# Kernel tuning notes

Measured on AMD Instinct MI355X. Metric: run time of the kernel, lower is better.

The kernel has to match this reference:

```python
import jax, jax.numpy as jnp
import numpy as np

B = 128      # graphs
N = 32       # atoms per graph (fixed)
NODES = B * N
E = B * N * N  # fully-connected edges incl. self-loops
H = 256      # hidden_dim
TD = 128     # time_dim
TYPE = 100   # type_dim
NF = 10      # frac_emb_freq
EDGE_DIM = NF * 2 * 3 + 6  # 66
L = 4        # num_layers
EPS = 1e-5


def _edges():
    idx = jnp.arange(NODES).reshape(B, N)
    ei = jnp.broadcast_to(idx[:, :, None], (B, N, N)).reshape(-1)  # row (target)
    ej = jnp.broadcast_to(idx[:, None, :], (B, N, N)).reshape(-1)  # col (source)
    return ei, ej


def _layernorm(x, g, b):
    mu = jnp.mean(x, axis=-1, keepdims=True)
    var = jnp.mean((x - mu) ** 2, axis=-1, keepdims=True)
    return (x - mu) * jax.lax.rsqrt(var + EPS) * g + b


def setup_inputs() -> dict:
    key = jax.random.key(0)
    ks = jax.random.split(key, 32)
    p = lambda k, shp: (jax.random.normal(k, shp, dtype=jnp.float32) * 0.02)
    inp = {
        "t": jax.random.uniform(ks[0], (B,), dtype=jnp.float32),
        "atom_types": jax.random.normal(ks[1], (NODES, TYPE), dtype=jnp.float32),
        "frac_coords": jax.random.uniform(ks[2], (NODES, 3), dtype=jnp.float32),
        "l_polar": jax.random.normal(ks[3], (B, 6), dtype=jnp.float32),
        "node2graph": jnp.repeat(jnp.arange(B, dtype=jnp.int32), N),
        # type_smooth
        "Ws": p(ks[4], (TYPE, H)), "bs": jnp.zeros((H,), jnp.float32),
        # node_embedding
        "Wn": p(ks[5], (H + TD, H)), "bn": jnp.zeros((H,), jnp.float32),
        # per-layer params, stacked over L
        "ln_g": jnp.ones((L, H), jnp.float32), "ln_b": jnp.zeros((L, H), jnp.float32),
        "m1_W": p(ks[6], (L, 2 * H + EDGE_DIM, H)), "m1_b": jnp.zeros((L, H), jnp.float32),
        "m2_W": p(ks[7], (L, H, H)), "m2_b": jnp.zeros((L, H), jnp.float32),
        "a1_W": p(ks[8], (L, 2 * H, H)), "a1_b": jnp.zeros((L, H), jnp.float32),
        "a2_W": p(ks[9], (L, H, H)), "a2_b": jnp.zeros((L, H), jnp.float32),
        # final layer norm + readouts
        "fln_g": jnp.ones((H,), jnp.float32), "fln_b": jnp.zeros((H,), jnp.float32),
        "type_W": p(ks[10], (H, TYPE)), "type_b": jnp.zeros((TYPE,), jnp.float32),
        "polar_W": p(ks[11], (H, 6)),
        "frac_W": p(ks[12], (H, 3)),
    }
    return inp


def reference(t, atom_types, frac_coords, l_polar, node2graph,
              Ws, bs, Wn, bn, ln_g, ln_b, m1_W, m1_b, m2_W, m2_b,
              a1_W, a1_b, a2_W, a2_b, fln_g, fln_b, type_W, type_b,
              polar_W, frac_W):
    ei, ej = _edges()
    edge2graph = node2graph[ei]

    # ---- node features: type_smooth + sinusoidal time embedding ----
    half = TD // 2
    tfreq = jnp.exp(jnp.arange(half, dtype=jnp.float32) * (-np.log(10000.0) / (half - 1)))
    targ = t[:, None] * tfreq[None, :]                       # [B, half]
    time_emb = jnp.concatenate([jnp.sin(targ), jnp.cos(targ)], axis=-1)  # [B, TD]
    time_emb = jnp.repeat(time_emb, N, axis=0)               # [NODES, TD]
    type_emb = atom_types @ Ws + bs                           # [NODES, H]
    nf = jnp.concatenate([type_emb, time_emb], axis=-1) @ Wn + bn  # [NODES, H]

    # ---- edge features: sinusoidal frac-diff embedding + l_polar ----
    d = jnp.mod(frac_coords[ej] - frac_coords[ei], 1.0)       # [E, 3]
    ffreq = 2.0 * np.pi * jnp.arange(NF, dtype=jnp.float32)
    femb = (d[:, :, None] * ffreq[None, None, :]).reshape(E, NF * 3)
    femb = jnp.concatenate([jnp.sin(femb), jnp.cos(femb)], axis=-1)  # [E, 60]
    ef = jnp.concatenate([femb, l_polar[edge2graph]], axis=-1)       # [E, 66]

    # ---- GNN layers ----
    ones = jnp.ones((E,), jnp.float32)
    cnt = jax.ops.segment_sum(ones, ei, num_segments=NODES)          # [NODES]
    cnt = jnp.maximum(cnt, 1.0)[:, None]
    for i in range(L):
        h = _layernorm(nf, ln_g[i], ln_b[i])
        mij = jnp.concatenate([h[ei], h[ej], ef], axis=-1)           # [E, 2H+66]
        mij = jax.nn.silu(mij @ m1_W[i] + m1_b[i])
        mij = jax.nn.silu(mij @ m2_W[i] + m2_b[i])                   # [E, H]
        msg = jax.ops.segment_sum(mij, ei, num_segments=NODES) / cnt  # scatter-mean
        a = jnp.concatenate([nf, msg], axis=-1)
        a = jax.nn.silu(a @ a1_W[i] + a1_b[i])
        a = jax.nn.silu(a @ a2_W[i] + a2_b[i])
        nf = nf + a

    nf = _layernorm(nf, fln_g, fln_b)
    gsum = jax.ops.segment_sum(nf, node2graph, num_segments=B)
    gcnt = jnp.maximum(jax.ops.segment_sum(jnp.ones((NODES,), jnp.float32), node2graph, num_segments=B), 1.0)
    graph_features = gsum / gcnt[:, None]

    type_pred = nf @ type_W + type_b
    l_polar_pred = graph_features @ polar_W
    frac_coords_pred = nf @ frac_W
    return type_pred, l_polar_pred, frac_coords_pred
```

## Files before the change

### kernel.cpp

```cpp
#include <hip/hip_runtime.h>
#include <hip/hip_bf16.h>

typedef __attribute__((ext_vector_type(8))) short short8;
typedef __attribute__((ext_vector_type(4))) short short4v;
typedef __attribute__((ext_vector_type(4))) float float4v;
typedef __bf16 bf16x8 __attribute__((ext_vector_type(8)));

#define MFMA16(A,B,C) __builtin_amdgcn_mfma_f32_16x16x32_bf16( \
    __builtin_bit_cast(bf16x8,(A)), __builtin_bit_cast(bf16x8,(B)), (C), 0, 0, 0)

static __device__ __forceinline__ float bf2f(unsigned short b){
  unsigned u = ((unsigned)b) << 16; float f; __builtin_memcpy(&f,&u,sizeof(f)); return f;
}
static __device__ __forceinline__ unsigned short f2bf(float f){
  __bf16 h = (__bf16)f;
  return __builtin_bit_cast(unsigned short, h);
}
static __device__ __forceinline__ float siluf(float x){
  return x * __builtin_amdgcn_rcpf(1.0f + __expf(-x));
}
static __device__ __forceinline__ float ldf(const float* p, size_t i){ return p[i]; }
static __device__ __forceinline__ float ldf(const unsigned short* p, size_t i){ return bf2f(p[i]); }

__global__ __launch_bounds__(256) void k_gemm(
    const unsigned short* __restrict__ A, int lda,
    const unsigned short* __restrict__ Bp, int KT, int NT,
    const float* __restrict__ bias,
    float* __restrict__ outF, int ldoF,
    unsigned short* __restrict__ outH, int ldoH,
    const float* __restrict__ res,
    int Nc, int flags)
{
  const int w = threadIdx.x >> 6, lane = threadIdx.x & 63;
  const int l15 = lane & 15, q = lane >> 4;
  const int rowL = blockIdx.x * 64 + w * 16;
  const int colB = blockIdx.y * 64;
  const short8* pa = (const short8*)(A + (size_t)(rowL + l15) * lda);
  const short8* pb = (const short8*)Bp;
  float4v acc[4] = {};
  int ntc[4];
  #pragma unroll
  for (int i = 0; i < 4; ++i){ int t = (colB >> 4) + i; ntc[i] = t < NT ? t : NT - 1; }
  for (int kt = 0; kt < KT; ++kt){
    short8 a = pa[kt * 4 + q];
    #pragma unroll
    for (int i = 0; i < 4; ++i){
      short8 b = pb[(size_t)(kt * NT + ntc[i]) * 64 + lane];
      acc[i] = MFMA16(a, b, acc[i]);
    }
  }
  const bool doB = flags & 2, doS = flags & 1, doR = flags & 4;
  #pragma unroll
  for (int i = 0; i < 4; ++i){
    int c = colB + i * 16 + l15;
    if (c >= Nc) continue;
    float bv = doB ? bias[c] : 0.0f;
    #pragma unroll
    for (int r = 0; r < 4; ++r){
      int row = rowL + q * 4 + r;
      float v = acc[i][r] + bv;
      if (doS) v = siluf(v);
      if (doR) v += res[(size_t)row * ldoF + c];
      if (outF) outF[(size_t)row * ldoF + c] = v;
      if (outH) outH[(size_t)row * ldoH + c] = f2bf(v);
    }
  }
}

template<typename T>
static __device__ __forceinline__ void pack_tile(
    const T* W, int ldw, int Krows, int Ncols,
    unsigned short* dst, int NTtot, int ntoff, int kt, int nt,
    const float* addrow)
{
  int lane = threadIdx.x;
  int l15 = lane & 15, q = lane >> 4;
  int col = nt * 16 + l15;
  int kr0 = kt * 32 + q * 8;
  short8 v;
  #pragma unroll
  for (int j = 0; j < 8; ++j){
    int r = kr0 + j;
    float x = 0.0f;
    if (r < Krows && col < Ncols){
      x = ldf(W, (size_t)r * ldw + col);
      if (addrow) x += addrow[(r >> 5) * 256 + col];
    }
    v[j] = (short)f2bf(x);
  }
  ((short8*)dst)[(size_t)(kt * NTtot + ntoff + nt) * 64 + lane] = v;
}

__global__ void k_packW(
    const float* Ws, const float* Wn,
    const float* typeW, const float* polarW, const float* fracW,
    const float* m1W, const float* m2W, const float* a1W, const float* a2W,
    unsigned short* Wsp, unsigned short* Wnp, unsigned short* typep,
    unsigned short* polarp, unsigned short* fracp,
    unsigned short* W12p, unsigned short* W1botp, unsigned short* W2Tp,
    unsigned short* a1p, unsigned short* a2p)
{
  int b = blockIdx.x;
  if (b < 64)      { pack_tile(Ws,    256, 100, 256, Wsp,   16, 0, b >> 4, b & 15, nullptr); return; }
  if (b < 256){ int s = b - 64;  pack_tile(Wn,    256, 384, 256, Wnp,   16, 0, s >> 4, s & 15, nullptr); return; }
  if (b < 312){ int s = b - 256; pack_tile(typeW, 100, 256, 100, typep,  7, 0, s / 7,  s % 7,  nullptr); return; }
  if (b < 320){ int s = b - 312; pack_tile(polarW,  6, 256,   6, polarp, 1, 0, s, 0, nullptr); return; }
  if (b < 328){ int s = b - 320; pack_tile(fracW,   3, 256,   3, fracp,  1, 0, s, 0, nullptr); return; }
  int s2 = b - 328;
  int l = s2 / 800, bb = s2 % 800;
  const float* m1Wl = m1W + (size_t)l * 578 * 256;
  const float* m2Wl = m2W + (size_t)l * 65536;
  const float* a1Wl = a1W + (size_t)l * 131072;
  const float* a2Wl = a2W + (size_t)l * 65536;
  unsigned short* W12pl   = W12p   + (size_t)l * 131072;
  unsigned short* W1botpl = W1botp + (size_t)l * 16384;
  unsigned short* W2Tpl   = W2Tp   + (size_t)l * 65536;
  unsigned short* a1pl    = a1p    + (size_t)l * 131072;
  unsigned short* a2pl    = a2p    + (size_t)l * 65536;
  if (bb < 128)       pack_tile(m1Wl,           256, 256, 256, W12pl,  32,  0, bb >> 4, bb & 15, nullptr);
  else if (bb < 256){ int s = bb - 128; pack_tile(m1Wl + 256*256, 256, 256, 256, W12pl,  32, 16, s >> 4, s & 15, nullptr); }
  else if (bb < 288){ int s = bb - 256; pack_tile(m1Wl + 512*256, 256,  64, 256, W1botpl,16,  0, s >> 4, s & 15, nullptr); }
  else if (bb < 416){ int s = bb - 288; pack_tile(m2Wl,           256, 256, 256, W2Tpl,  16,  0, s >> 4, s & 15, nullptr); }
  else if (bb < 672){ int s = bb - 416; pack_tile(a1Wl,           256, 512, 256, a1pl,   16,  0, s >> 4, s & 15, nullptr); }
  else              { int s = bb - 672; pack_tile(a2Wl,           256, 256, 256, a2pl,   16,  0, s >> 4, s & 15, nullptr); }
}

__global__ void k_prep2(const float* at, const float* t, const float* fc,
                        const float* lpol, const float* m1W, const float* m1b,
                        unsigned short* atp, unsigned short* cat1,
                        unsigned short* femb, float* lpw)
{
  int b = blockIdx.x;
  if (b < 2048){
    int id = b * 256 + threadIdx.x;
    int r = id >> 7, c = id & 127;
    atp[id] = (c < 100) ? f2bf(at[r * 100 + c]) : (unsigned short)0;
  } else if (b < 2176){
    int g = b - 2048, i = threadIdx.x;
    if (i < 128){
      float tg = t[g];
      int f = i & 63;
      float fr = __expf((-9.210340371976184f / 63.0f) * (float)f);
      float arg = tg * fr;
      float v = (i < 64) ? __sinf(arg) : __cosf(arg);
      unsigned short hv = f2bf(v);
      for (int n = 0; n < 32; ++n)
        cat1[(size_t)(g * 32 + n) * 384 + 256 + i] = hv;
    }
  } else if (b < 2688){
    int e = (b - 2176) * 256 + threadIdx.x;
    int g = e >> 10, i = (e >> 5) & 31, j = e & 31;
    int nt = g * 32 + i, ns = g * 32 + j;
    unsigned short o[64];
    #pragma unroll
    for (int k = 0; k < 3; ++k){
      float d = fc[ns * 3 + k] - fc[nt * 3 + k];
      d -= floorf(d);
      #pragma unroll
      for (int f = 0; f < 10; ++f){
        float ang = d * (6.283185307179586f * (float)f);
        o[k * 10 + f]      = f2bf(__sinf(ang));
        o[30 + k * 10 + f] = f2bf(__cosf(ang));
      }
    }
    #pragma unroll
    for (int z = 60; z < 64; ++z) o[z] = 0;
    short8* dst = (short8*)(femb + (size_t)e * 64);
    #pragma unroll
    for (int v = 0; v < 8; ++v){
      short8 s;
      #pragma unroll
      for (int j2 = 0; j2 < 8; ++j2) s[j2] = (short)o[v * 8 + j2];
      dst[v] = s;
    }
  } else {
    int s = b - 2688;
    int l = s >> 7, g = s & 127, c = threadIdx.x;
    const float* W = m1W + (size_t)l * 578 * 256;
    float acc = m1b[l * 256 + c];
    #pragma unroll
    for (int k = 0; k < 6; ++k)
      acc += lpol[g * 6 + k] * W[(572 + k) * 256 + c];
    lpw[((size_t)l * 128 + g) * 256 + c] = acc;
  }
}

#define HLD 264

__global__ __launch_bounds__(256) void k_lnP(
    const float* __restrict__ nf, const float* __restrict__ g_,
    const float* __restrict__ b_,
    const unsigned short* __restrict__ W12p, const float* __restrict__ lpwl,
    unsigned short* __restrict__ P1, unsigned short* __restrict__ P2)
{
  __shared__ unsigned short hld[32 * HLD];
  const int w = threadIdx.x >> 6, lane = threadIdx.x & 63;
  const int l15 = lane & 15, q = lane >> 4;
  const int g = blockIdx.x >> 1, halfT = blockIdx.x & 1;
  #pragma unroll
  for (int rr = 0; rr < 8; ++rr){
    int row = w * 8 + rr;
    float4v x = *(const float4v*)(nf + ((size_t)(g*32+row))*256 + lane*4);
    float s = x[0]+x[1]+x[2]+x[3];
    #pragma unroll
    for (int m=1;m<64;m<<=1) s += __shfl_xor(s,m,64);
    float mu = s * (1.f/256.f);
    float d0=x[0]-mu,d1=x[1]-mu,d2=x[2]-mu,d3=x[3]-mu;
    float vs=d0*d0+d1*d1+d2*d2+d3*d3;
    #pragma unroll
    for (int m=1;m<64;m<<=1) vs += __shfl_xor(vs,m,64);
    float rs = rsqrtf(vs*(1.f/256.f)+1e-5f);
    float4v gg = *(const float4v*)(g_ + lane*4);
    float4v bb = *(const float4v*)(b_ + lane*4);
    short4v o;
    o[0]=(short)f2bf(d0*rs*gg[0]+bb[0]);
    o[1]=(short)f2bf(d1*rs*gg[1]+bb[1]);
    o[2]=(short)f2bf(d2*rs*gg[2]+bb[2]);
    o[3]=(short)f2bf(d3*rs*gg[3]+bb[3]);
    *(short4v*)(&hld[row*HLD + lane*4]) = o;
  }
  __syncthreads();
  float4v acc[2][4] = {};
  const short8* pb = (const short8*)W12p;
  for (int kt = 0; kt < 8; ++kt){
    short8 a0 = *(const short8*)(&hld[(size_t)l15*HLD + kt*32 + q*8]);
    short8 a1 = *(const short8*)(&hld[(size_t)(16+l15)*HLD + kt*32 + q*8]);
    #pragma unroll
    for (int i = 0; i < 4; ++i){
      short8 bfr = pb[(size_t)(kt*32 + halfT*16 + w*4 + i)*64 + lane];
      acc[0][i] = MFMA16(a0, bfr, acc[0][i]);
      acc[1][i] = MFMA16(a1, bfr, acc[1][i]);
    }
  }
  unsigned short* dst = halfT ? P2 : P1;
  #pragma unroll
  for (int i = 0; i < 4; ++i){
    int ch = (w*4 + i)*16 + l15;
    float lv = (halfT == 0) ? lpwl[g*256 + ch] : 0.0f;
    #pragma unroll
    for (int mt = 0; mt < 2; ++mt){
      #pragma unroll
      for (int r = 0; r < 4; ++r){
        int node = g*32 + mt*16 + q*4 + r;
        dst[(size_t)node*256 + ch] = f2bf(acc[mt][i][r] + lv);
      }
    }
  }
}

__global__ __launch_bounds__(256) void k_a12(
    const unsigned short* __restrict__ cat2,
    const unsigned short* __restrict__ a1pl, const float* __restrict__ a1bl,
    const unsigned short* __restrict__ a2pl, const float* __restrict__ a2bl,
    float* __restrict__ nf, unsigned short* __restrict__ cat2w)
{
  __shared__ unsigned short t1[16 * HLD];
  const int w = threadIdx.x >> 6, lane = threadIdx.x & 63;
  const int l15 = lane & 15, q = lane >> 4;
  const int r0 = blockIdx.x * 16;
  const short8* pb1 = (const short8*)a1pl;
  const short8* pb2 = (const short8*)a2pl;
  float4v acc[4] = {};
  for (int kt = 0; kt < 16; ++kt){
    short8 a0 = *(const short8*)(cat2 + (size_t)(r0 + l15)*512 + kt*32 + q*8);
    #pragma unroll
    for (int i = 0; i < 4; ++i){
      short8 bfr = pb1[(size_t)(kt*16 + w*4 + i)*64 + lane];
      acc[i] = MFMA16(a0, bfr, acc[i]);
    }
  }
  #pragma unroll
  for (int i = 0; i < 4; ++i){
    int c = (w*4+i)*16 + l15;
    float bv = a1bl[c];
    #pragma unroll
    for (int r = 0; r < 4; ++r)
      t1[(size_t)(q*4 + r)*HLD + c] = f2bf(siluf(acc[i][r] + bv));
  }
  __syncthreads();
  float4v c2[4] = {};
  for (int kt = 0; kt < 8; ++kt){
    short8 a0 = *(const short8*)(&t1[(size_t)l15*HLD + kt*32 + q*8]);
    #pragma unroll
    for (int i = 0; i < 4; ++i){
      short8 bfr = pb2[(size_t)(kt*16 + w*4 + i)*64 + lane];
      c2[i] = MFMA16(a0, bfr, c2[i]);
    }
  }
  #pragma unroll
  for (int i = 0; i < 4; ++i){
    int c = (w*4+i)*16 + l15;
    float bv = a2bl[c];
    #pragma unroll
    for (int r = 0; r < 4; ++r){
      int row = r0 + q*4 + r;
      float v = nf[(size_t)row*256 + c] + siluf(c2[i][r] + bv);
      nf[(size_t)row*256 + c] = v;
      cat2w[(size_t)row*512 + c] = f2bf(v);
    }
  }
}

__global__ __launch_bounds__(256) void k_lnF(
    const float* __restrict__ nf, const float* __restrict__ g_,
    const float* __restrict__ b_,
    unsigned short* __restrict__ h, unsigned short* __restrict__ gf)
{
  __shared__ unsigned short hld[32 * HLD];
  const int w = threadIdx.x >> 6, lane = threadIdx.x & 63;
  const int g = blockIdx.x;
  #pragma unroll
  for (int rr = 0; rr < 8; ++rr){
    int row = w * 8 + rr;
    float4v x = *(const float4v*)(nf + ((size_t)(g*32+row))*256 + lane*4);
    float s = x[0]+x[1]+x[2]+x[3];
    #pragma unroll
    for (int m=1;m<64;m<<=1) s += __shfl_xor(s,m,64);
    float mu = s * (1.f/256.f);
    float d0=x[0]-mu,d1=x[1]-mu,d2=x[2]-mu,d3=x[3]-mu;
    float vs=d0*d0+d1*d1+d2*d2+d3*d3;
    #pragma unroll
    for (int m=1;m<64;m<<=1) vs += __shfl_xor(vs,m,64);
    float rs = rsqrtf(vs*(1.f/256.f)+1e-5f);
    float4v gg = *(const float4v*)(g_ + lane*4);
    float4v bb = *(const float4v*)(b_ + lane*4);
    short4v o;
    o[0]=(short)f2bf(d0*rs*gg[0]+bb[0]);
    o[1]=(short)f2bf(d1*rs*gg[1]+bb[1]);
    o[2]=(short)f2bf(d2*rs*gg[2]+bb[2]);
    o[3]=(short)f2bf(d3*rs*gg[3]+bb[3]);
    *(short4v*)(&hld[row*HLD + lane*4]) = o;
    *(short4v*)(h + ((size_t)(g*32+row))*256 + lane*4) = o;
  }
  __syncthreads();
  int c = threadIdx.x;
  float s = 0.0f;
  #pragma unroll
  for (int n = 0; n < 32; ++n) s += bf2f(hld[n*HLD + c]);
  gf[g*256 + c] = f2bf(s * (1.0f/32.0f));
}

#define EST 268
__global__ __launch_bounds__(256, 4) void k_edge(
    const unsigned short* __restrict__ femb,
    const unsigned short* __restrict__ W1botp,
    const unsigned short* __restrict__ P1,
    const unsigned short* __restrict__ P2,
    const unsigned short* __restrict__ W2Tp,
    const float* __restrict__ b2,
    unsigned short* __restrict__ cat2)
{
  __shared__ unsigned short M1[64 * EST];
  const int w = threadIdx.x >> 6, lane = threadIdx.x & 63;
  const int l15 = lane & 15, q = lane >> 4;
  const int b = blockIdx.x, g = b >> 4;
  const int n0 = (b & 15) * 2;
  const int cb = w * 64;
  const short8* fb8  = (const short8*)femb;
  const short8* w1b8 = (const short8*)W1botp;
  const short8* w2t8 = (const short8*)W2Tp;

  short4v p1v[2][4], p2v[2][4];
  #pragma unroll
  for (int ct = 0; ct < 4; ++ct){
    int co = cb + ct*16 + q*4;
    p1v[0][ct] = *(const short4v*)(P1 + (size_t)(g*32 + n0    )*256 + co);
    p1v[1][ct] = *(const short4v*)(P1 + (size_t)(g*32 + n0 + 1)*256 + co);
    p2v[0][ct] = *(const short4v*)(P2 + (size_t)(g*32 +      l15)*256 + co);
    p2v[1][ct] = *(const short4v*)(P2 + (size_t)(g*32 + 16 + l15)*256 + co);
  }

  float4v acc[4][4] = {};
  #pragma unroll
  for (int ks = 0; ks < 2; ++ks){
    short8 a[4];
    #pragma unroll
    for (int ct = 0; ct < 4; ++ct)
      a[ct] = w1b8[(size_t)(ks * 16 + w * 4 + ct) * 64 + lane];
    #pragma unroll
    for (int et = 0; et < 4; ++et){
      int edge = b * 64 + et * 16 + l15;
      short8 bf = fb8[(size_t)edge * 8 + ks * 4 + q];
      #pragma unroll
      for (int ct = 0; ct < 4; ++ct)
        acc[ct][et] = MFMA16(a[ct], bf, acc[ct][et]);
    }
  }
  #pragma unroll
  for (int ct = 0; ct < 4; ++ct)
    #pragma unroll
    for (int et = 0; et < 4; ++et){
      short4v sv;
      #pragma unroll
      for (int r = 0; r < 4; ++r){
        float v = acc[ct][et][r] + bf2f(p1v[et>>1][ct][r]) + bf2f(p2v[et&1][ct][r]);
        sv[r] = (short)f2bf(siluf(v));
      }
      *(short4v*)(&M1[(size_t)(et * 16 + l15) * EST + cb + ct * 16 + q * 4]) = sv;
    }
  __syncthreads();
  float4v c2[4][4] = {};
  for (int kt = 0; kt < 8; ++kt){
    short8 a[4];
    #pragma unroll
    for (int ct = 0; ct < 4; ++ct)
      a[ct] = w2t8[(size_t)(kt * 16 + w * 4 + ct) * 64 + lane];
    #pragma unroll
    for (int et = 0; et < 4; ++et){
      short8 m = *(const short8*)(&M1[(size_t)(et * 16 + l15) * EST + kt * 32 + q * 8]);
      #pragma unroll
      for (int ct = 0; ct < 4; ++ct)
        c2[ct][et] = MFMA16(m, a[ct], c2[ct][et]);
    }
  }
  #pragma unroll
  for (int ct = 0; ct < 4; ++ct){
    float bv = b2[cb + ct * 16 + l15];
    #pragma unroll
    for (int nn = 0; nn < 2; ++nn){
      float s = siluf(c2[ct][2*nn  ][0] + bv) + siluf(c2[ct][2*nn  ][1] + bv)
              + siluf(c2[ct][2*nn  ][2] + bv) + siluf(c2[ct][2*nn  ][3] + bv)
              + siluf(c2[ct][2*nn+1][0] + bv) + siluf(c2[ct][2*nn+1][1] + bv)
              + siluf(c2[ct][2*nn+1][2] + bv) + siluf(c2[ct][2*nn+1][3] + bv);
      s += __shfl_xor(s, 16, 64);
      s += __shfl_xor(s, 32, 64);
      if (q == 0)
        cat2[(size_t)(b*2 + nn) * 512 + 256 + cb + ct * 16 + l15] =
            f2bf(s * (1.0f / 32.0f));
    }
  }
}

extern "C" void kernel_launch(void* const* d_in, const int* in_sizes, int n_in,
                              void* d_out, int out_size, void* d_ws, size_t ws_size,
                              hipStream_t stream)
{
  const float* t      = (const float*)d_in[0];
  const float* at     = (const float*)d_in[1];
  const float* fc     = (const float*)d_in[2];
  const float* lpol   = (const float*)d_in[3];
  const float* Ws     = (const float*)d_in[5];
  const float* bs     = (const float*)d_in[6];
  const float* Wn     = (const float*)d_in[7];
  const float* bn     = (const float*)d_in[8];
  const float* ln_g   = (const float*)d_in[9];
  const float* ln_b   = (const float*)d_in[10];
  const float* m1W    = (const float*)d_in[11];
  const float* m1b    = (const float*)d_in[12];
  const float* m2W    = (const float*)d_in[13];
  const float* m2b    = (const float*)d_in[14];
  const float* a1W    = (const float*)d_in[15];
  const float* a1b    = (const float*)d_in[16];
  const float* a2W    = (const float*)d_in[17];
  const float* a2b    = (const float*)d_in[18];
  const float* flng   = (const float*)d_in[19];
  const float* flnb   = (const float*)d_in[20];
  const float* typeW  = (const float*)d_in[21];
  const float* typeb  = (const float*)d_in[22];
  const float* polarW = (const float*)d_in[23];
  const float* fracW  = (const float*)d_in[24];
  float* out = (float*)d_out;

  char* ws = (char*)d_ws;
  size_t off = 0;
  auto alloc = [&](size_t bytes) -> char* {
    char* p = ws + off; off += (bytes + 255) & ~(size_t)255; return p;
  };
  float*          nf    = (float*)         alloc((size_t)4096*256*4);
  unsigned short* cat2  = (unsigned short*)alloc((size_t)4096*512*2);
  unsigned short* h     = (unsigned short*)alloc((size_t)4096*256*2);
  unsigned short* cat1  = (unsigned short*)alloc((size_t)4096*384*2);
  unsigned short* atp   = (unsigned short*)alloc((size_t)4096*128*2);
  unsigned short* femb  = (unsigned short*)alloc((size_t)131072*64*2);
  float*          lpw   = (float*)         alloc((size_t)4*128*256*4);
  unsigned short* P1    = (unsigned short*)alloc((size_t)4096*256*2);
  unsigned short* P2    = (unsigned short*)alloc((size_t)4096*256*2);
  unsigned short* gf    = (unsigned short*)alloc((size_t)128*256*2);
  unsigned short* Wsp   = (unsigned short*)alloc((size_t)4*16*1024);
  unsigned short* Wnp   = (unsigned short*)alloc((size_t)12*16*1024);
  unsigned short* typep = (unsigned short*)alloc((size_t)8*7*1024);
  unsigned short* polarp= (unsigned short*)alloc((size_t)8*1*1024);
  unsigned short* fracp = (unsigned short*)alloc((size_t)8*1*1024);
  unsigned short* W12p  = (unsigned short*)alloc((size_t)4*131072*2);
  unsigned short* W1botp= (unsigned short*)alloc((size_t)4*16384*2);
  unsigned short* W2Tp  = (unsigned short*)alloc((size_t)4*65536*2);
  unsigned short* a1p   = (unsigned short*)alloc((size_t)4*131072*2);
  unsigned short* a2p   = (unsigned short*)alloc((size_t)4*65536*2);

  k_packW<<<dim3(3528), dim3(64), 0, stream>>>(Ws, Wn, typeW, polarW, fracW,
      m1W, m2W, a1W, a2W,
      Wsp, Wnp, typep, polarp, fracp, W12p, W1botp, W2Tp, a1p, a2p);
  k_prep2<<<dim3(3200), dim3(256), 0, stream>>>(at, t, fc, lpol, m1W, m1b,
                                                atp, cat1, femb, lpw);
  k_gemm<<<dim3(64,4), dim3(256), 0, stream>>>(atp, 128, Wsp, 4, 16, bs,
      (float*)nullptr, 0, cat1, 384, (const float*)nullptr, 256, 2);
  k_gemm<<<dim3(64,4), dim3(256), 0, stream>>>(cat1, 384, Wnp, 12, 16, bn,
      nf, 256, cat2, 512, (const float*)nullptr, 256, 2);

  for (int l = 0; l < 4; ++l){
    k_lnP<<<dim3(256), dim3(256), 0, stream>>>(nf, ln_g + l*256, ln_b + l*256,
        W12p + (size_t)l*131072, lpw + (size_t)l*32768, P1, P2);
    k_edge<<<dim3(2048), dim3(256), 0, stream>>>(femb, W1botp + (size_t)l*16384,
        P1, P2, W2Tp + (size_t)l*65536, m2b + l*256, cat2);
    k_a12<<<dim3(256), dim3(256), 0, stream>>>(cat2, a1p + (size_t)l*131072,
        a1b + l*256, a2p + (size_t)l*65536, a2b + l*256, nf, cat2);
  }

  k_lnF<<<dim3(128), dim3(256), 0, stream>>>(nf, flng, flnb, h, gf);
  k_gemm<<<dim3(64,2), dim3(256), 0, stream>>>(h, 256, typep, 8, 7, typeb,
      out, 100, (unsigned short*)nullptr, 0, (const float*)nullptr, 100, 2);
  k_gemm<<<dim3(2,1), dim3(256), 0, stream>>>(gf, 256, polarp, 8, 1,
      (const float*)nullptr, out + 409600, 6, (unsigned short*)nullptr, 0,
      (const float*)nullptr, 6, 0);
  k_gemm<<<dim3(64,1), dim3(256), 0, stream>>>(h, 256, fracp, 8, 1,
      (const float*)nullptr, out + 410368, 3, (unsigned short*)nullptr, 0,
      (const float*)nullptr, 3, 0);
}
```

Before: 374.3 us.

## Merge prep and output launches, split lnP/a12 work across more blocks

Weight packing and input prep now run in one 256-thread kernel, with four 64-lane pack tiles per block. The three readout GEMMs are merged into one multi-role kernel. This removes three kernel launches and their serialization gaps. k_lnP and k_a12 now split their output columns across twice as many blocks (512 instead of 256), which raises occupancy on the many-CU GPU. The cost is that the LayerNorm and first GEMM are computed redundantly in each extra block.

```diff
diff --git a/kernel.cpp b/kernel.cpp
--- a/kernel.cpp
+++ b/kernel.cpp
@@ -21,6 +21,51 @@
 }
 static __device__ __forceinline__ float ldf(const float* p, size_t i){ return p[i]; }
 static __device__ __forceinline__ float ldf(const unsigned short* p, size_t i){ return bf2f(p[i]); }
+
+static __device__ __forceinline__ void gemm_body(
+    const unsigned short* __restrict__ A, int lda,
+    const unsigned short* __restrict__ Bp, int KT, int NT,
+    const float* __restrict__ bias,
+    float* __restrict__ outF, int ldoF,
+    unsigned short* __restrict__ outH, int ldoH,
+    const float* __restrict__ res,
+    int Nc, int flags, int bx, int by)
+{
+  const int w = threadIdx.x >> 6, lane = threadIdx.x & 63;
+  const int l15 = lane & 15, q = lane >> 4;
+  const int rowL = bx * 64 + w * 16;
+  const int colB = by * 64;
+  const short8* pa = (const short8*)(A + (size_t)(rowL + l15) * lda);
+  const short8* pb = (const short8*)Bp;
+  float4v acc[4] = {};
+  int ntc[4];
+  #pragma unroll
+  for (int i = 0; i < 4; ++i){ int t = (colB >> 4) + i; ntc[i] = t < NT ? t : NT - 1; }
+  for (int kt = 0; kt < KT; ++kt){
+    short8 a = pa[kt * 4 + q];
+    #pragma unroll
+    for (int i = 0; i < 4; ++i){
+      short8 b = pb[(size_t)(kt * NT + ntc[i]) * 64 + lane];
+      acc[i] = MFMA16(a, b, acc[i]);
+    }
+  }
+  const bool doB = flags & 2, doS = flags & 1, doR = flags & 4;
+  #pragma unroll
+  for (int i = 0; i < 4; ++i){
+    int c = colB + i * 16 + l15;
+    if (c >= Nc) continue;
+    float bv = doB ? bias[c] : 0.0f;
+    #pragma unroll
+    for (int r = 0; r < 4; ++r){
+      int row = rowL + q * 4 + r;
+      float v = acc[i][r] + bv;
+      if (doS) v = siluf(v);
+      if (doR) v += res[(size_t)row * ldoF + c];
+      if (outF) outF[(size_t)row * ldoF + c] = v;
+      if (outH) outH[(size_t)row * ldoH + c] = f2bf(v);
+    }
+  }
+}
 
 __global__ __launch_bounds__(256) void k_gemm(
     const unsigned short* __restrict__ A, int lda,
@@ -31,39 +76,29 @@
     const float* __restrict__ res,
     int Nc, int flags)
 {
-  const int w = threadIdx.x >> 6, lane = threadIdx.x & 63;
-  const int l15 = lane & 15, q = lane >> 4;
-  const int rowL = blockIdx.x * 64 + w * 16;
-  const int colB = blockIdx.y * 64;
-  const short8* pa = (const short8*)(A + (size_t)(rowL + l15) * lda);
-  const short8* pb = (const short8*)Bp;
-  float4v acc[4] = {};
-  int ntc[4];
-  #pragma unroll
-  for (int i = 0; i < 4; ++i){ int t = (colB >> 4) + i; ntc[i] = t < NT ? t : NT - 1; }
-  for (int kt = 0; kt < KT; ++kt){
-    short8 a = pa[kt * 4 + q];
-    #pragma unroll
-    for (int i = 0; i < 4; ++i){
-      short8 b = pb[(size_t)(kt * NT + ntc[i]) * 64 + lane];
-      acc[i] = MFMA16(a, b, acc[i]);
-    }
-  }
-  const bool doB = flags & 2, doS = flags & 1, doR = flags & 4;
-  #pragma unroll
-  for (int i = 0; i < 4; ++i){
-    int c = colB + i * 16 + l15;
-    if (c >= Nc) continue;
-    float bv = doB ? bias[c] : 0.0f;
-    #pragma unroll
-    for (int r = 0; r < 4; ++r){
-      int row = rowL + q * 4 + r;
-      float v = acc[i][r] + bv;
-      if (doS) v = siluf(v);
-      if (doR) v += res[(size_t)row * ldoF + c];
-      if (outF) outF[(size_t)row * ldoF + c] = v;
-      if (outH) outH[(size_t)row * ldoH + c] = f2bf(v);
-    }
+  gemm_body(A, lda, Bp, KT, NT, bias, outF, ldoF, outH, ldoH, res, Nc, flags,
+            blockIdx.x, blockIdx.y);
+}
+
+__global__ __launch_bounds__(256) void k_out(
+    const unsigned short* __restrict__ h, const unsigned short* __restrict__ gf,
+    const unsigned short* __restrict__ typep, const float* __restrict__ typeb,
+    const unsigned short* __restrict__ polarp, const unsigned short* __restrict__ fracp,
+    float* __restrict__ out)
+{
+  int b = blockIdx.x;
+  if (b < 128){
+    gemm_body(h, 256, typep, 8, 7, typeb, out, 100,
+              (unsigned short*)nullptr, 0, (const float*)nullptr, 100, 2,
+              b & 63, b >> 6);
+  } else if (b < 130){
+    gemm_body(gf, 256, polarp, 8, 1, (const float*)nullptr, out + 409600, 6,
+              (unsigned short*)nullptr, 0, (const float*)nullptr, 6, 0,
+              b - 128, 0);
+  } else {
+    gemm_body(h, 256, fracp, 8, 1, (const float*)nullptr, out + 410368, 3,
+              (unsigned short*)nullptr, 0, (const float*)nullptr, 3, 0,
+              b - 130, 0);
   }
 }
 
@@ -71,9 +106,8 @@
 static __device__ __forceinline__ void pack_tile(
     const T* W, int ldw, int Krows, int Ncols,
     unsigned short* dst, int NTtot, int ntoff, int kt, int nt,
-    const float* addrow)
-{
-  int lane = threadIdx.x;
+    const float* addrow, int lane)
+{
   int l15 = lane & 15, q = lane >> 4;
   int col = nt * 16 + l15;
   int kr0 = kt * 32 + q * 8;
@@ -91,7 +125,8 @@
   ((short8*)dst)[(size_t)(kt * NTtot + ntoff + nt) * 64 + lane] = v;
 }
 
-__global__ void k_packW(
+static __device__ __forceinline__ void packW_dispatch(
+    int b, int lane,
     const float* Ws, const float* Wn,
     const float* typeW, const float* polarW, const float* fracW,
     const float* m1W, const float* m2W, const float* a1W, const float* a2W,
@@ -100,12 +135,11 @@
     unsigned short* W12p, unsigned short* W1botp, unsigned short* W2Tp,
     unsigned short* a1p, unsigned short* a2p)
 {
-  int b = blockIdx.x;
-  if (b < 64)      { pack_tile(Ws,    256, 100, 256, Wsp,   16, 0, b >> 4, b & 15, nullptr); return; }
-  if (b < 256){ int s = b - 64;  pack_tile(Wn,    256, 384, 256, Wnp,   16, 0, s >> 4, s & 15, nullptr); return; }
-  if (b < 312){ int s = b - 256; pack_tile(typeW, 100, 256, 100, typep,  7, 0, s / 7,  s % 7,  nullptr); return; }
-  if (b < 320){ int s = b - 312; pack_tile(polarW,  6, 256,   6, polarp, 1, 0, s, 0, nullptr); return; }
-  if (b < 328){ int s = b - 320; pack_tile(fracW,   3, 256,   3, fracp,  1, 0, s, 0, nullptr); return; }
+  if (b < 64)      { pack_tile(Ws,    256, 100, 256, Wsp,   16, 0, b >> 4, b & 15, nullptr, lane); return; }
+  if (b < 256){ int s = b - 64;  pack_tile(Wn,    256, 384, 256, Wnp,   16, 0, s >> 4, s & 15, nullptr, lane); return; }
+  if (b < 312){ int s = b - 256; pack_tile(typeW, 100, 256, 100, typep,  7, 0, s / 7,  s % 7,  nullptr, lane); return; }
+  if (b < 320){ int s = b - 312; pack_tile(polarW,  6, 256,   6, polarp, 1, 0, s, 0, nullptr, lane); return; }
+  if (b < 328){ int s = b - 320; pack_tile(fracW,   3, 256,   3, fracp,  1, 0, s, 0, nullptr, lane); return; }
   int s2 = b - 328;
   int l = s2 / 800, bb = s2 % 800;
   const float* m1Wl = m1W + (size_t)l * 578 * 256;
@@ -117,20 +151,36 @@
   unsigned short* W2Tpl   = W2Tp   + (size_t)l * 65536;
   unsigned short* a1pl    = a1p    + (size_t)l * 131072;
   unsigned short* a2pl    = a2p    + (size_t)l * 65536;
-  if (bb < 128)       pack_tile(m1Wl,           256, 256, 256, W12pl,  32,  0, bb >> 4, bb & 15, nullptr);
-  else if (bb < 256){ int s = bb - 128; pack_tile(m1Wl + 256*256, 256, 256, 256, W12pl,  32, 16, s >> 4, s & 15, nullptr); }
-  else if (bb < 288){ int s = bb - 256; pack_tile(m1Wl + 512*256, 256,  64, 256, W1botpl,16,  0, s >> 4, s & 15, nullptr); }
-  else if (bb < 416){ int s = bb - 288; pack_tile(m2Wl,           256, 256, 256, W2Tpl,  16,  0, s >> 4, s & 15, nullptr); }
-  else if (bb < 672){ int s = bb - 416; pack_tile(a1Wl,           256, 512, 256, a1pl,   16,  0, s >> 4, s & 15, nullptr); }
-  else              { int s = bb - 672; pack_tile(a2Wl,           256, 256, 256, a2pl,   16,  0, s >> 4, s & 15, nullptr); }
-}
-
-__global__ void k_prep2(const float* at, const float* t, const float* fc,
-                        const float* lpol, const float* m1W, const float* m1b,
-                        unsigned short* atp, unsigned short* cat1,
-                        unsigned short* femb, float* lpw)
-{
-  int b = blockIdx.x;
+  if (bb < 128)       pack_tile(m1Wl,           256, 256, 256, W12pl,  32,  0, bb >> 4, bb & 15, nullptr, lane);
+  else if (bb < 256){ int s = bb - 128; pack_tile(m1Wl + 256*256, 256, 256, 256, W12pl,  32, 16, s >> 4, s & 15, nullptr, lane); }
+  else if (bb < 288){ int s = bb - 256; pack_tile(m1Wl + 512*256, 256,  64, 256, W1botpl,16,  0, s >> 4, s & 15, nullptr, lane); }
+  else if (bb < 416){ int s = bb - 288; pack_tile(m2Wl,           256, 256, 256, W2Tpl,  16,  0, s >> 4, s & 15, nullptr, lane); }
+  else if (bb < 672){ int s = bb - 416; pack_tile(a1Wl,           256, 512, 256, a1pl,   16,  0, s >> 4, s & 15, nullptr, lane); }
+  else              { int s = bb - 672; pack_tile(a2Wl,           256, 256, 256, a2pl,   16,  0, s >> 4, s & 15, nullptr, lane); }
+}
+
+__global__ void k_prep(
+    const float* Ws, const float* Wn,
+    const float* typeW, const float* polarW, const float* fracW,
+    const float* m1W, const float* m2W, const float* a1W, const float* a2W,
+    unsigned short* Wsp, unsigned short* Wnp, unsigned short* typep,
+    unsigned short* polarp, unsigned short* fracp,
+    unsigned short* W12p, unsigned short* W1botp, unsigned short* W2Tp,
+    unsigned short* a1p, unsigned short* a2p,
+    const float* at, const float* t, const float* fc,
+    const float* lpol, const float* m1b,
+    unsigned short* atp, unsigned short* cat1,
+    unsigned short* femb, float* lpw)
+{
+  int b0 = blockIdx.x;
+  if (b0 < 882){
+    int tile = b0 * 4 + (threadIdx.x >> 6);
+    packW_dispatch(tile, threadIdx.x & 63, Ws, Wn, typeW, polarW, fracW,
+                   m1W, m2W, a1W, a2W, Wsp, Wnp, typep, polarp, fracp,
+                   W12p, W1botp, W2Tp, a1p, a2p);
+    return;
+  }
+  int b = b0 - 882;
   if (b < 2048){
     int id = b * 256 + threadIdx.x;
     int r = id >> 7, c = id & 127;
@@ -196,7 +246,7 @@
   __shared__ unsigned short hld[32 * HLD];
   const int w = threadIdx.x >> 6, lane = threadIdx.x & 63;
   const int l15 = lane & 15, q = lane >> 4;
-  const int g = blockIdx.x >> 1, halfT = blockIdx.x & 1;
+  const int g = blockIdx.x >> 2, q4 = blockIdx.x & 3;
   #pragma unroll
   for (int rr = 0; rr < 8; ++rr){
     int row = w * 8 + rr;
@@ -220,23 +270,24 @@
     *(short4v*)(&hld[row*HLD + lane*4]) = o;
   }
   __syncthreads();
-  float4v acc[2][4] = {};
+  float4v acc[2][2] = {};
   const short8* pb = (const short8*)W12p;
   for (int kt = 0; kt < 8; ++kt){
     short8 a0 = *(const short8*)(&hld[(size_t)l15*HLD + kt*32 + q*8]);
     short8 a1 = *(const short8*)(&hld[(size_t)(16+l15)*HLD + kt*32 + q*8]);
     #pragma unroll
-    for (int i = 0; i < 4; ++i){
-      short8 bfr = pb[(size_t)(kt*32 + halfT*16 + w*4 + i)*64 + lane];
+    for (int i = 0; i < 2; ++i){
+      short8 bfr = pb[(size_t)(kt*32 + q4*8 + w*2 + i)*64 + lane];
       acc[0][i] = MFMA16(a0, bfr, acc[0][i]);
       acc[1][i] = MFMA16(a1, bfr, acc[1][i]);
     }
   }
-  unsigned short* dst = halfT ? P2 : P1;
-  #pragma unroll
-  for (int i = 0; i < 4; ++i){
-    int ch = (w*4 + i)*16 + l15;
-    float lv = (halfT == 0) ? lpwl[g*256 + ch] : 0.0f;
+  unsigned short* dst = (q4 < 2) ? P1 : P2;
+  const int cho = (q4 & 1) * 128;
+  #pragma unroll
+  for (int i = 0; i < 2; ++i){
+    int ch = cho + (w*2 + i)*16 + l15;
+    float lv = (q4 < 2) ? lpwl[g*256 + ch] : 0.0f;
     #pragma unroll
     for (int mt = 0; mt < 2; ++mt){
       #pragma unroll
@@ -257,7 +308,7 @@
   __shared__ unsigned short t1[16 * HLD];
   const int w = threadIdx.x >> 6, lane = threadIdx.x & 63;
   const int l15 = lane & 15, q = lane >> 4;
-  const int r0 = blockIdx.x * 16;
+  const int r0 = (blockIdx.x >> 1) * 16, h2 = blockIdx.x & 1;
   const short8* pb1 = (const short8*)a1pl;
   const short8* pb2 = (const short8*)a2pl;
   float4v acc[4] = {};
@@ -278,18 +329,18 @@
       t1[(size_t)(q*4 + r)*HLD + c] = f2bf(siluf(acc[i][r] + bv));
   }
   __syncthreads();
-  float4v c2[4] = {};
+  float4v c2[2] = {};
   for (int kt = 0; kt < 8; ++kt){
     short8 a0 = *(const short8*)(&t1[(size_t)l15*HLD + kt*32 + q*8]);
     #pragma unroll
-    for (int i = 0; i < 4; ++i){
-      short8 bfr = pb2[(size_t)(kt*16 + w*4 + i)*64 + lane];
+    for (int i = 0; i < 2; ++i){
+      short8 bfr = pb2[(size_t)(kt*16 + h2*8 + w*2 + i)*64 + lane];
       c2[i] = MFMA16(a0, bfr, c2[i]);
     }
   }
   #pragma unroll
-  for (int i = 0; i < 4; ++i){
-    int c = (w*4+i)*16 + l15;
+  for (int i = 0; i < 2; ++i){
+    int c = h2*128 + (w*2+i)*16 + l15;
     float bv = a2bl[c];
     #pragma unroll
     for (int r = 0; r < 4; ++r){
@@ -487,32 +538,25 @@
   unsigned short* a1p   = (unsigned short*)alloc((size_t)4*131072*2);
   unsigned short* a2p   = (unsigned short*)alloc((size_t)4*65536*2);
 
-  k_packW<<<dim3(3528), dim3(64), 0, stream>>>(Ws, Wn, typeW, polarW, fracW,
+  k_prep<<<dim3(4082), dim3(256), 0, stream>>>(Ws, Wn, typeW, polarW, fracW,
       m1W, m2W, a1W, a2W,
-      Wsp, Wnp, typep, polarp, fracp, W12p, W1botp, W2Tp, a1p, a2p);
-  k_prep2<<<dim3(3200), dim3(256), 0, stream>>>(at, t, fc, lpol, m1W, m1b,
-                                                atp, cat1, femb, lpw);
+      Wsp, Wnp, typep, polarp, fracp, W12p, W1botp, W2Tp, a1p, a2p,
+      at, t, fc, lpol, m1b, atp, cat1, femb, lpw);
   k_gemm<<<dim3(64,4), dim3(256), 0, stream>>>(atp, 128, Wsp, 4, 16, bs,
       (float*)nullptr, 0, cat1, 384, (const float*)nullptr, 256, 2);
   k_gemm<<<dim3(64,4), dim3(256), 0, stream>>>(cat1, 384, Wnp, 12, 16, bn,
       nf, 256, cat2, 512, (const float*)nullptr, 256, 2);
 
   for (int l = 0; l < 4; ++l){
-    k_lnP<<<dim3(256), dim3(256), 0, stream>>>(nf, ln_g + l*256, ln_b + l*256,
+    k_lnP<<<dim3(512), dim3(256), 0, stream>>>(nf, ln_g + l*256, ln_b + l*256,
         W12p + (size_t)l*131072, lpw + (size_t)l*32768, P1, P2);
     k_edge<<<dim3(2048), dim3(256), 0, stream>>>(femb, W1botp + (size_t)l*16384,
         P1, P2, W2Tp + (size_t)l*65536, m2b + l*256, cat2);
-    k_a12<<<dim3(256), dim3(256), 0, stream>>>(cat2, a1p + (size_t)l*131072,
+    k_a12<<<dim3(512), dim3(256), 0, stream>>>(cat2, a1p + (size_t)l*131072,
         a1b + l*256, a2p + (size_t)l*65536, a2b + l*256, nf, cat2);
   }
 
   k_lnF<<<dim3(128), dim3(256), 0, stream>>>(nf, flng, flnb, h, gf);
-  k_gemm<<<dim3(64,2), dim3(256), 0, stream>>>(h, 256, typep, 8, 7, typeb,
-      out, 100, (unsigned short*)nullptr, 0, (const float*)nullptr, 100, 2);
-  k_gemm<<<dim3(2,1), dim3(256), 0, stream>>>(gf, 256, polarp, 8, 1,
-      (const float*)nullptr, out + 409600, 6, (unsigned short*)nullptr, 0,
-      (const float*)nullptr, 6, 0);
-  k_gemm<<<dim3(64,1), dim3(256), 0, stream>>>(h, 256, fracp, 8, 1,
-      (const float*)nullptr, out + 410368, 3, (unsigned short*)nullptr, 0,
-      (const float*)nullptr, 3, 0);
-}
+  k_out<<<dim3(194), dim3(256), 0, stream>>>(h, gf, typep, typeb,
+                                             polarp, fracp, out);
+}
```

After: 366.9 us. 2.0% less time.
